# Kernel optimization log

Hardware: AMD Instinct MI355X
Metric: run time of the kernel (lower is better)

The kernel has to match this reference:

```python
import jax, jax.numpy as jnp
import numpy as np

IN_FEATS = 602
N_HIDDEN = 256
N_CLASSES = 41
N_SRC0 = 292864   # block-1 src nodes (2-hop neighborhood)
N_DST0 = 11264    # block-1 dst == block-0 src (1-hop neighborhood)
N_DST1 = 1024     # seeds
FAN0 = 25         # neighbors per dst in block applied by layer 0
FAN1 = 10         # neighbors per dst in block applied by layer 1


def setup_inputs() -> dict:
    key = jax.random.key(0)
    ks = jax.random.split(key, 9)
    x = jax.random.normal(ks[0], (N_SRC0, IN_FEATS), dtype=jnp.float32)
    src_idx0 = jax.random.randint(ks[1], (N_DST0 * FAN0,), 0, N_SRC0)
    src_idx1 = jax.random.randint(ks[2], (N_DST1 * FAN1,), 0, N_DST0)
    s0 = 1.0 / np.sqrt(IN_FEATS)
    s1 = 1.0 / np.sqrt(N_HIDDEN)
    W_self0 = jax.random.uniform(ks[3], (IN_FEATS, N_HIDDEN), jnp.float32, -s0, s0)
    W_neigh0 = jax.random.uniform(ks[4], (IN_FEATS, N_HIDDEN), jnp.float32, -s0, s0)
    b0 = jnp.zeros((N_HIDDEN,), jnp.float32)
    W_self1 = jax.random.uniform(ks[5], (N_HIDDEN, N_CLASSES), jnp.float32, -s1, s1)
    W_neigh1 = jax.random.uniform(ks[6], (N_HIDDEN, N_CLASSES), jnp.float32, -s1, s1)
    b1 = jnp.zeros((N_CLASSES,), jnp.float32)
    return {"x": x, "W_self0": W_self0, "W_neigh0": W_neigh0, "b0": b0,
            "W_self1": W_self1, "W_neigh1": W_neigh1, "b1": b1,
            "src_idx0": src_idx0, "src_idx1": src_idx1}


def _sage_layer(h_src, h_dst, src_idx, fanout, W_self, W_neigh, b):
    # mean aggregation over exactly `fanout` sampled neighbors per dst node
    n_dst = h_dst.shape[0]
    h_neigh = h_src[src_idx].reshape(n_dst, fanout, -1).mean(axis=1)
    return h_dst @ W_self + h_neigh @ W_neigh + b


def reference(x, W_self0, W_neigh0, b0, W_self1, W_neigh1, b1, src_idx0, src_idx1):
    # layer 0: [N_SRC0, in] -> [N_DST0, hidden], relu; dropout is identity (eval mode)
    h = jax.nn.relu(_sage_layer(x, x[:N_DST0], src_idx0, FAN0, W_self0, W_neigh0, b0))
    # layer 1: [N_DST0, hidden] -> [N_DST1, classes], no activation
    out = _sage_layer(h, h[:N_DST1], src_idx1, FAN1, W_self1, W_neigh1, b1)
    return out
```

## Files before the change

### kernel.cpp

```cpp
#include <hip/hip_runtime.h>
#include <hip/hip_bf16.h>

#define IN_FEATS 602
#define N_HIDDEN 256
#define N_CLASSES 41
#define N_SRC0 292864
#define N_DST0 11264
#define N_DST1 1024
#define FAN0 25
#define FAN1 10
#define KPAD 1216

typedef __attribute__((ext_vector_type(4))) float f32x4;
typedef __attribute__((ext_vector_type(8))) short bf16x8;

static __device__ __forceinline__ unsigned pack_bf16x2(float lo, float hi) {
    unsigned a = __float_as_uint(lo);
    unsigned b = __float_as_uint(hi);
    a = (a + 0x7fffu + ((a >> 16) & 1u)) >> 16;
    b = (b + 0x7fffu + ((b >> 16) & 1u)) >> 16;
    return (a & 0xffffu) | (b << 16);
}

__global__ __launch_bounds__(256) void agg0_kernel(
    const float* __restrict__ x,
    const int* __restrict__ idx,
    __hip_bfloat16* __restrict__ A)
{
    const int wave = threadIdx.x >> 6;
    const int lane = threadIdx.x & 63;
    const int d = blockIdx.x * 4 + wave;

    __shared__ int sidx[4][FAN0];
    if (lane < FAN0) sidx[wave][lane] = idx[d * FAN0 + lane];
    __syncthreads();

    unsigned* Aself  = (unsigned*)(A + (size_t)d * KPAD);
    const float* xself = x + (size_t)d * IN_FEATS;

    if (lane < 6) Aself[602 + lane] = 0u;

    #pragma unroll
    for (int p = 0; p < 5; ++p) {
        const int f2 = p * 64 + lane;
        if (f2 > 300) break;
        const int f = f2 * 2;
        float sx = 0.f, sy = 0.f;
        #pragma unroll
        for (int n = 0; n < FAN0; ++n) {
            const float2 v = *(const float2*)&x[(size_t)sidx[wave][n] * IN_FEATS + f];
            sx += v.x; sy += v.y;
        }
        const float2 s = *(const float2*)&xself[f];
        Aself[f2] = pack_bf16x2(s.x, s.y);
        ((unsigned*)((__hip_bfloat16*)Aself + IN_FEATS))[f2] =
            pack_bf16x2(sx * (1.0f / FAN0), sy * (1.0f / FAN0));
    }
}

__global__ __launch_bounds__(256) void wprep_kernel(
    const float* __restrict__ Ws,
    const float* __restrict__ Wn,
    __hip_bfloat16* __restrict__ Wt)
{
    __shared__ float tile[32][33];
    const int k0 = blockIdx.x * 32, n0 = blockIdx.y * 32;
    const int tx = threadIdx.x & 31, ty = threadIdx.x >> 5;

    #pragma unroll
    for (int i = 0; i < 4; ++i) {
        const int k = k0 + ty + i * 8;
        const int n = n0 + tx;
        float v = 0.f;
        if (k < IN_FEATS)            v = Ws[(size_t)k * N_HIDDEN + n];
        else if (k < 2 * IN_FEATS)   v = Wn[(size_t)(k - IN_FEATS) * N_HIDDEN + n];
        tile[ty + i * 8][tx] = v;
    }
    __syncthreads();
    #pragma unroll
    for (int i = 0; i < 4; ++i) {
        const int n = n0 + ty + i * 8;
        const int k = k0 + tx;
        Wt[(size_t)n * KPAD + k] = __float2bfloat16(tile[tx][ty + i * 8]);
    }
}

#define BKK 64
#define LDSW 72

__global__ __launch_bounds__(256) void gemm0_mfma(
    const __hip_bfloat16* __restrict__ A,
    const __hip_bfloat16* __restrict__ Wt,
    const float* __restrict__ bias,
    float* __restrict__ h)
{
    __shared__ __hip_bfloat16 As[64 * LDSW];
    __shared__ __hip_bfloat16 Bs[64 * LDSW];

    const int tid  = threadIdx.x;
    const int lane = tid & 63;
    const int wave = tid >> 6;
    const int wm = wave >> 1, wn = wave & 1;
    const int g = lane >> 4, r = lane & 15;
    const int m0 = blockIdx.y * 64, n0 = blockIdx.x * 64;

    const int srow = tid >> 2;
    const int sc   = (tid & 3) * 16;

    const size_t a_off = (size_t)(m0 + srow) * KPAD + sc;
    const size_t b_off = (size_t)(n0 + srow) * KPAD + sc;

    f32x4 acc[2][2] = {};

    for (int k0 = 0; k0 < KPAD; k0 += BKK) {
        *(float4*)&As[srow * LDSW + sc]     = *(const float4*)&A[a_off + k0];
        *(float4*)&As[srow * LDSW + sc + 8] = *(const float4*)&A[a_off + k0 + 8];
        *(float4*)&Bs[srow * LDSW + sc]     = *(const float4*)&Wt[b_off + k0];
        *(float4*)&Bs[srow * LDSW + sc + 8] = *(const float4*)&Wt[b_off + k0 + 8];
        __syncthreads();

        #pragma unroll
        for (int kh = 0; kh < 2; ++kh) {
            const bf16x8 af0 = *(const bf16x8*)&As[(wm * 32 +      r) * LDSW + kh * 32 + g * 8];
            const bf16x8 af1 = *(const bf16x8*)&As[(wm * 32 + 16 + r) * LDSW + kh * 32 + g * 8];
            const bf16x8 bf0 = *(const bf16x8*)&Bs[(wn * 32 +      r) * LDSW + kh * 32 + g * 8];
            const bf16x8 bf1 = *(const bf16x8*)&Bs[(wn * 32 + 16 + r) * LDSW + kh * 32 + g * 8];

            acc[0][0] = __builtin_amdgcn_mfma_f32_16x16x32_bf16(af0, bf0, acc[0][0], 0, 0, 0);
            acc[0][1] = __builtin_amdgcn_mfma_f32_16x16x32_bf16(af0, bf1, acc[0][1], 0, 0, 0);
            acc[1][0] = __builtin_amdgcn_mfma_f32_16x16x32_bf16(af1, bf0, acc[1][0], 0, 0, 0);
            acc[1][1] = __builtin_amdgcn_mfma_f32_16x16x32_bf16(af1, bf1, acc[1][1], 0, 0, 0);
        }
        __syncthreads();
    }

    #pragma unroll
    for (int mh = 0; mh < 2; ++mh)
        #pragma unroll
        for (int nh = 0; nh < 2; ++nh) {
            const int col = n0 + wn * 32 + nh * 16 + r;
            const float bv = bias[col];
            #pragma unroll
            for (int j = 0; j < 4; ++j) {
                const int row = m0 + wm * 32 + mh * 16 + g * 4 + j;
                const float v = acc[mh][nh][j] + bv;
                h[(size_t)row * N_HIDDEN + col] = fmaxf(v, 0.f);
            }
        }
}

__global__ __launch_bounds__(64) void tail_kernel(
    const float* __restrict__ h,
    const int* __restrict__ idx1,
    const float* __restrict__ Ws,
    const float* __restrict__ Wn,
    const float* __restrict__ b,
    float* __restrict__ out)
{
    const int d = blockIdx.x;
    __shared__ float hd[N_HIDDEN];
    __shared__ float hn[N_HIDDEN];
    __shared__ int sidx[FAN1];
    if (threadIdx.x < FAN1) sidx[threadIdx.x] = idx1[d * FAN1 + threadIdx.x];
    __syncthreads();

    for (int k = threadIdx.x; k < N_HIDDEN; k += 64) {
        hd[k] = h[(size_t)d * N_HIDDEN + k];
        float a = 0.f;
        #pragma unroll
        for (int i = 0; i < FAN1; ++i)
            a += h[(size_t)sidx[i] * N_HIDDEN + k];
        hn[k] = a * (1.0f / FAN1);
    }
    __syncthreads();

    if (threadIdx.x < N_CLASSES) {
        const int n = threadIdx.x;
        float a0 = b[n], a1 = 0.f, a2 = 0.f, a3 = 0.f;
        #pragma unroll 4
        for (int k = 0; k < N_HIDDEN; k += 4) {
            a0 += hd[k + 0] * Ws[(k + 0) * N_CLASSES + n] + hn[k + 0] * Wn[(k + 0) * N_CLASSES + n];
            a1 += hd[k + 1] * Ws[(k + 1) * N_CLASSES + n] + hn[k + 1] * Wn[(k + 1) * N_CLASSES + n];
            a2 += hd[k + 2] * Ws[(k + 2) * N_CLASSES + n] + hn[k + 2] * Wn[(k + 2) * N_CLASSES + n];
            a3 += hd[k + 3] * Ws[(k + 3) * N_CLASSES + n] + hn[k + 3] * Wn[(k + 3) * N_CLASSES + n];
        }
        out[(size_t)d * N_CLASSES + n] = a0 + a1 + a2 + a3;
    }
}

extern "C" void kernel_launch(void* const* d_in, const int* in_sizes, int n_in,
                              void* d_out, int out_size, void* d_ws, size_t ws_size,
                              hipStream_t stream) {
    const float* x       = (const float*)d_in[0];
    const float* Wself0  = (const float*)d_in[1];
    const float* Wneigh0 = (const float*)d_in[2];
    const float* b0      = (const float*)d_in[3];
    const float* Wself1  = (const float*)d_in[4];
    const float* Wneigh1 = (const float*)d_in[5];
    const float* b1      = (const float*)d_in[6];
    const int*   idx0    = (const int*)d_in[7];
    const int*   idx1    = (const int*)d_in[8];
    float* out = (float*)d_out;

    __hip_bfloat16* Abf = (__hip_bfloat16*)d_ws;
    __hip_bfloat16* Wt  = Abf + (size_t)N_DST0 * KPAD;
    float*          h   = (float*)(Wt + (size_t)N_HIDDEN * KPAD);

    wprep_kernel<<<dim3(KPAD / 32, N_HIDDEN / 32), 256, 0, stream>>>(Wself0, Wneigh0, Wt);
    agg0_kernel<<<N_DST0 / 4, 256, 0, stream>>>(x, idx0, Abf);
    gemm0_mfma<<<dim3(N_HIDDEN / 64, N_DST0 / 64), 256, 0, stream>>>(Abf, Wt, b0, h);
    tail_kernel<<<N_DST1, 64, 0, stream>>>(h, idx1, Wself1, Wneigh1, b1, out);
}
```

Measured before the change: 231.3 us.

## Fuse neighbor aggregation into layer-0 GEMM via LDS-resident A tile

Merges the gather/mean aggregation kernel and the MFMA GEMM into one kernel. Each block aggregates 16 destination rows into an LDS bf16 tile, then each wave computes 64 output columns, streaming the weight fragments directly from global memory with register double-buffering. This removes the round trip of the bf16 A matrix through global memory and one launch. In exchange, every block re-reads the full 1216x256 weight matrix from L2, and 704 blocks each doing serial gather work may limit latency hiding.

```diff
diff --git a/kernel.cpp b/kernel.cpp
--- a/kernel.cpp
+++ b/kernel.cpp
@@ -10,6 +10,8 @@
 #define FAN0 25
 #define FAN1 10
 #define KPAD 1216
+#define MT 16
+#define ALDS 1224
 
 typedef __attribute__((ext_vector_type(4))) float f32x4;
 typedef __attribute__((ext_vector_type(8))) short bf16x8;
@@ -20,42 +22,6 @@
     a = (a + 0x7fffu + ((a >> 16) & 1u)) >> 16;
     b = (b + 0x7fffu + ((b >> 16) & 1u)) >> 16;
     return (a & 0xffffu) | (b << 16);
-}
-
-__global__ __launch_bounds__(256) void agg0_kernel(
-    const float* __restrict__ x,
-    const int* __restrict__ idx,
-    __hip_bfloat16* __restrict__ A)
-{
-    const int wave = threadIdx.x >> 6;
-    const int lane = threadIdx.x & 63;
-    const int d = blockIdx.x * 4 + wave;
-
-    __shared__ int sidx[4][FAN0];
-    if (lane < FAN0) sidx[wave][lane] = idx[d * FAN0 + lane];
-    __syncthreads();
-
-    unsigned* Aself  = (unsigned*)(A + (size_t)d * KPAD);
-    const float* xself = x + (size_t)d * IN_FEATS;
-
-    if (lane < 6) Aself[602 + lane] = 0u;
-
-    #pragma unroll
-    for (int p = 0; p < 5; ++p) {
-        const int f2 = p * 64 + lane;
-        if (f2 > 300) break;
-        const int f = f2 * 2;
-        float sx = 0.f, sy = 0.f;
-        #pragma unroll
-        for (int n = 0; n < FAN0; ++n) {
-            const float2 v = *(const float2*)&x[(size_t)sidx[wave][n] * IN_FEATS + f];
-            sx += v.x; sy += v.y;
-        }
-        const float2 s = *(const float2*)&xself[f];
-        Aself[f2] = pack_bf16x2(s.x, s.y);
-        ((unsigned*)((__hip_bfloat16*)Aself + IN_FEATS))[f2] =
-            pack_bf16x2(sx * (1.0f / FAN0), sy * (1.0f / FAN0));
-    }
 }
 
 __global__ __launch_bounds__(256) void wprep_kernel(
@@ -85,68 +51,91 @@
     }
 }
 
-#define BKK 64
-#define LDSW 72
-
-__global__ __launch_bounds__(256) void gemm0_mfma(
-    const __hip_bfloat16* __restrict__ A,
+__global__ __launch_bounds__(256) void fused0_kernel(
+    const float* __restrict__ x,
+    const int* __restrict__ idx0,
     const __hip_bfloat16* __restrict__ Wt,
     const float* __restrict__ bias,
     float* __restrict__ h)
 {
-    __shared__ __hip_bfloat16 As[64 * LDSW];
-    __shared__ __hip_bfloat16 Bs[64 * LDSW];
+    __shared__ __hip_bfloat16 Atile[MT][ALDS];
 
     const int tid  = threadIdx.x;
     const int lane = tid & 63;
-    const int wave = tid >> 6;
-    const int wm = wave >> 1, wn = wave & 1;
-    const int g = lane >> 4, r = lane & 15;
-    const int m0 = blockIdx.y * 64, n0 = blockIdx.x * 64;
-
-    const int srow = tid >> 2;
-    const int sc   = (tid & 3) * 16;
-
-    const size_t a_off = (size_t)(m0 + srow) * KPAD + sc;
-    const size_t b_off = (size_t)(n0 + srow) * KPAD + sc;
-
-    f32x4 acc[2][2] = {};
-
-    for (int k0 = 0; k0 < KPAD; k0 += BKK) {
-        *(float4*)&As[srow * LDSW + sc]     = *(const float4*)&A[a_off + k0];
-        *(float4*)&As[srow * LDSW + sc + 8] = *(const float4*)&A[a_off + k0 + 8];
-        *(float4*)&Bs[srow * LDSW + sc]     = *(const float4*)&Wt[b_off + k0];
-        *(float4*)&Bs[srow * LDSW + sc + 8] = *(const float4*)&Wt[b_off + k0 + 8];
-        __syncthreads();
-
-        #pragma unroll
-        for (int kh = 0; kh < 2; ++kh) {
-            const bf16x8 af0 = *(const bf16x8*)&As[(wm * 32 +      r) * LDSW + kh * 32 + g * 8];
-            const bf16x8 af1 = *(const bf16x8*)&As[(wm * 32 + 16 + r) * LDSW + kh * 32 + g * 8];
-            const bf16x8 bf0 = *(const bf16x8*)&Bs[(wn * 32 +      r) * LDSW + kh * 32 + g * 8];
-            const bf16x8 bf1 = *(const bf16x8*)&Bs[(wn * 32 + 16 + r) * LDSW + kh * 32 + g * 8];
-
-            acc[0][0] = __builtin_amdgcn_mfma_f32_16x16x32_bf16(af0, bf0, acc[0][0], 0, 0, 0);
-            acc[0][1] = __builtin_amdgcn_mfma_f32_16x16x32_bf16(af0, bf1, acc[0][1], 0, 0, 0);
-            acc[1][0] = __builtin_amdgcn_mfma_f32_16x16x32_bf16(af1, bf0, acc[1][0], 0, 0, 0);
-            acc[1][1] = __builtin_amdgcn_mfma_f32_16x16x32_bf16(af1, bf1, acc[1][1], 0, 0, 0);
-        }
-        __syncthreads();
-    }
-
-    #pragma unroll
-    for (int mh = 0; mh < 2; ++mh)
-        #pragma unroll
-        for (int nh = 0; nh < 2; ++nh) {
-            const int col = n0 + wn * 32 + nh * 16 + r;
-            const float bv = bias[col];
-            #pragma unroll
-            for (int j = 0; j < 4; ++j) {
-                const int row = m0 + wm * 32 + mh * 16 + g * 4 + j;
-                const float v = acc[mh][nh][j] + bv;
-                h[(size_t)row * N_HIDDEN + col] = fmaxf(v, 0.f);
+    const int w    = tid >> 6;
+    const int r    = lane & 15;
+    const int g    = lane >> 4;
+
+    #pragma unroll
+    for (int s = 0; s < 4; ++s) {
+        const int local = w * 4 + s;
+        const int d = blockIdx.x * MT + local;
+        const int* ip = idx0 + d * FAN0;
+
+        int ridx[FAN0];
+        #pragma unroll
+        for (int n = 0; n < FAN0; ++n)
+            ridx[n] = __builtin_amdgcn_readfirstlane(ip[n]);
+
+        if (lane < 10)
+            *(unsigned*)((char*)&Atile[local][0] + 2408 + lane * 4) = 0u;
+
+        #pragma unroll
+        for (int p = 0; p < 5; ++p) {
+            const int f2 = p * 64 + lane;
+            if (f2 <= 300) {
+                const int f = f2 * 2;
+                float sx = 0.f, sy = 0.f;
+                #pragma unroll
+                for (int n = 0; n < FAN0; ++n) {
+                    const float2 v = *(const float2*)&x[(size_t)ridx[n] * IN_FEATS + f];
+                    sx += v.x; sy += v.y;
+                }
+                const float2 sv = *(const float2*)&x[(size_t)d * IN_FEATS + f];
+                *(unsigned*)((char*)&Atile[local][0] + f2 * 4) = pack_bf16x2(sv.x, sv.y);
+                *(unsigned*)((char*)&Atile[local][0] + 1204 + f2 * 4) =
+                    pack_bf16x2(sx * (1.0f / FAN0), sy * (1.0f / FAN0));
             }
         }
+    }
+    __syncthreads();
+
+    const int cb = w * 64;
+    f32x4 acc[4] = {};
+
+#define LOADB(T, B) { _Pragma("unroll") \
+    for (int nf = 0; nf < 4; ++nf) \
+        B[nf] = *(const bf16x8*)&Wt[(size_t)(cb + nf * 16 + r) * KPAD + (T) * 32 + g * 8]; }
+#define DOMFMA(T, B) { \
+    const bf16x8 af = *(const bf16x8*)&Atile[r][(T) * 32 + g * 8]; \
+    _Pragma("unroll") \
+    for (int nf = 0; nf < 4; ++nf) \
+        acc[nf] = __builtin_amdgcn_mfma_f32_16x16x32_bf16(af, B[nf], acc[nf], 0, 0, 0); }
+
+    bf16x8 bA[4], bB[4];
+    LOADB(0, bA)
+    for (int t = 0; t < 36; t += 2) {
+        LOADB(t + 1, bB)
+        DOMFMA(t, bA)
+        LOADB(t + 2, bA)
+        DOMFMA(t + 1, bB)
+    }
+    LOADB(37, bB)
+    DOMFMA(36, bA)
+    DOMFMA(37, bB)
+#undef LOADB
+#undef DOMFMA
+
+    #pragma unroll
+    for (int nf = 0; nf < 4; ++nf) {
+        const int col = cb + nf * 16 + r;
+        const float bv = bias[col];
+        #pragma unroll
+        for (int j = 0; j < 4; ++j) {
+            const int row = blockIdx.x * MT + g * 4 + j;
+            h[(size_t)row * N_HIDDEN + col] = fmaxf(acc[nf][j] + bv, 0.f);
+        }
+    }
 }
 
 __global__ __launch_bounds__(64) void tail_kernel(
@@ -202,12 +191,10 @@
     const int*   idx1    = (const int*)d_in[8];
     float* out = (float*)d_out;
 
-    __hip_bfloat16* Abf = (__hip_bfloat16*)d_ws;
-    __hip_bfloat16* Wt  = Abf + (size_t)N_DST0 * KPAD;
-    float*          h   = (float*)(Wt + (size_t)N_HIDDEN * KPAD);
+    __hip_bfloat16* Wt = (__hip_bfloat16*)d_ws;
+    float*          h  = (float*)(Wt + (size_t)N_HIDDEN * KPAD);
 
     wprep_kernel<<<dim3(KPAD / 32, N_HIDDEN / 32), 256, 0, stream>>>(Wself0, Wneigh0, Wt);
-    agg0_kernel<<<N_DST0 / 4, 256, 0, stream>>>(x, idx0, Abf);
-    gemm0_mfma<<<dim3(N_HIDDEN / 64, N_DST0 / 64), 256, 0, stream>>>(Abf, Wt, b0, h);
+    fused0_kernel<<<N_DST0 / MT, 256, 0, stream>>>(x, idx0, Wt, b0, h);
     tail_kernel<<<N_DST1, 64, 0, stream>>>(h, idx1, Wself1, Wneigh1, b1, out);
 }
```

Result: slower. 243.2 us (+5.1%).

## Overlap chunked aggregation with GEMM via role-dispatched combo kernel

Applied to the files above, without the earlier changes.

Splits the layer-0 destination nodes into four chunks and launches a combined kernel whose blocks either prep weights, run the MFMA GEMM on the previous chunk, or aggregate the next chunk. The memory-bound gather then runs concurrently with the compute-bound GEMM in a software pipeline across launches. The tail kernel is also repacked to four destinations per 256-thread block with float4 gathers. The cost is extra launches and a shared LDS buffer sized for the largest role, which may reduce occupancy for the aggregation blocks.

```diff
diff --git a/kernel.cpp b/kernel.cpp
--- a/kernel.cpp
+++ b/kernel.cpp
@@ -10,6 +10,12 @@
 #define FAN0 25
 #define FAN1 10
 #define KPAD 1216
+#define LDSW 72
+#define NCHUNK 4
+#define CH (N_DST0 / NCHUNK)
+#define NW ((KPAD / 32) * 8)
+#define NGC (4 * (CH / 64))
+#define NAC (CH / 4)
 
 typedef __attribute__((ext_vector_type(4))) float f32x4;
 typedef __attribute__((ext_vector_type(8))) short bf16x8;
@@ -22,49 +28,16 @@
     return (a & 0xffffu) | (b << 16);
 }
 
-__global__ __launch_bounds__(256) void agg0_kernel(
-    const float* __restrict__ x,
-    const int* __restrict__ idx,
-    __hip_bfloat16* __restrict__ A)
-{
-    const int wave = threadIdx.x >> 6;
-    const int lane = threadIdx.x & 63;
-    const int d = blockIdx.x * 4 + wave;
-
-    __shared__ int sidx[4][FAN0];
-    if (lane < FAN0) sidx[wave][lane] = idx[d * FAN0 + lane];
-    __syncthreads();
-
-    unsigned* Aself  = (unsigned*)(A + (size_t)d * KPAD);
-    const float* xself = x + (size_t)d * IN_FEATS;
-
-    if (lane < 6) Aself[602 + lane] = 0u;
-
-    #pragma unroll
-    for (int p = 0; p < 5; ++p) {
-        const int f2 = p * 64 + lane;
-        if (f2 > 300) break;
-        const int f = f2 * 2;
-        float sx = 0.f, sy = 0.f;
-        #pragma unroll
-        for (int n = 0; n < FAN0; ++n) {
-            const float2 v = *(const float2*)&x[(size_t)sidx[wave][n] * IN_FEATS + f];
-            sx += v.x; sy += v.y;
-        }
-        const float2 s = *(const float2*)&xself[f];
-        Aself[f2] = pack_bf16x2(s.x, s.y);
-        ((unsigned*)((__hip_bfloat16*)Aself + IN_FEATS))[f2] =
-            pack_bf16x2(sx * (1.0f / FAN0), sy * (1.0f / FAN0));
-    }
-}
-
-__global__ __launch_bounds__(256) void wprep_kernel(
-    const float* __restrict__ Ws,
-    const float* __restrict__ Wn,
+#define SMBYTES (2 * 64 * LDSW * 2)
+
+static __device__ __forceinline__ void wprep_role(
+    int b, char* sm,
+    const float* __restrict__ Ws, const float* __restrict__ Wn,
     __hip_bfloat16* __restrict__ Wt)
 {
-    __shared__ float tile[32][33];
-    const int k0 = blockIdx.x * 32, n0 = blockIdx.y * 32;
+    float (*tile)[33] = (float(*)[33])sm;
+    const int k0 = (b % (KPAD / 32)) * 32;
+    const int n0 = (b / (KPAD / 32)) * 32;
     const int tx = threadIdx.x & 31, ty = threadIdx.x >> 5;
 
     #pragma unroll
@@ -85,24 +58,61 @@
     }
 }
 
-#define BKK 64
-#define LDSW 72
-
-__global__ __launch_bounds__(256) void gemm0_mfma(
+static __device__ __forceinline__ void agg_role(
+    int b, int dst0, char* sm,
+    const float* __restrict__ x,
+    const int* __restrict__ idx0,
+    __hip_bfloat16* __restrict__ A)
+{
+    int (*sidx)[FAN0] = (int(*)[FAN0])sm;
+    const int wave = threadIdx.x >> 6;
+    const int lane = threadIdx.x & 63;
+    const int d = dst0 + b * 4 + wave;
+
+    if (lane < FAN0) sidx[wave][lane] = idx0[d * FAN0 + lane];
+    __syncthreads();
+
+    unsigned* Aself = (unsigned*)(A + (size_t)d * KPAD);
+    const float* xself = x + (size_t)d * IN_FEATS;
+
+    if (lane < 6) Aself[602 + lane] = 0u;
+
+    #pragma unroll
+    for (int p = 0; p < 5; ++p) {
+        const int f2 = p * 64 + lane;
+        if (f2 <= 300) {
+            const int f = f2 * 2;
+            float sx = 0.f, sy = 0.f;
+            #pragma unroll
+            for (int n = 0; n < FAN0; ++n) {
+                const float2 v = *(const float2*)&x[(size_t)sidx[wave][n] * IN_FEATS + f];
+                sx += v.x; sy += v.y;
+            }
+            const float2 sv = *(const float2*)&xself[f];
+            *(unsigned*)((char*)Aself + f2 * 4) = pack_bf16x2(sv.x, sv.y);
+            *(unsigned*)((char*)Aself + 1204 + f2 * 4) =
+                pack_bf16x2(sx * (1.0f / FAN0), sy * (1.0f / FAN0));
+        }
+    }
+}
+
+static __device__ __forceinline__ void gemm_role(
+    int b, int dst0, char* sm,
     const __hip_bfloat16* __restrict__ A,
     const __hip_bfloat16* __restrict__ Wt,
     const float* __restrict__ bias,
     float* __restrict__ h)
 {
-    __shared__ __hip_bfloat16 As[64 * LDSW];
-    __shared__ __hip_bfloat16 Bs[64 * LDSW];
+    short* As = (short*)sm;
+    short* Bs = As + 64 * LDSW;
 
     const int tid  = threadIdx.x;
     const int lane = tid & 63;
     const int wave = tid >> 6;
     const int wm = wave >> 1, wn = wave & 1;
     const int g = lane >> 4, r = lane & 15;
-    const int m0 = blockIdx.y * 64, n0 = blockIdx.x * 64;
+    const int n0 = (b & 3) * 64;
+    const int m0 = dst0 + (b >> 2) * 64;
 
     const int srow = tid >> 2;
     const int sc   = (tid & 3) * 16;
@@ -112,7 +122,7 @@
 
     f32x4 acc[2][2] = {};
 
-    for (int k0 = 0; k0 < KPAD; k0 += BKK) {
+    for (int k0 = 0; k0 < KPAD; k0 += 64) {
         *(float4*)&As[srow * LDSW + sc]     = *(const float4*)&A[a_off + k0];
         *(float4*)&As[srow * LDSW + sc + 8] = *(const float4*)&A[a_off + k0 + 8];
         *(float4*)&Bs[srow * LDSW + sc]     = *(const float4*)&Wt[b_off + k0];
@@ -143,13 +153,32 @@
             #pragma unroll
             for (int j = 0; j < 4; ++j) {
                 const int row = m0 + wm * 32 + mh * 16 + g * 4 + j;
-                const float v = acc[mh][nh][j] + bv;
-                h[(size_t)row * N_HIDDEN + col] = fmaxf(v, 0.f);
+                h[(size_t)row * N_HIDDEN + col] = fmaxf(acc[mh][nh][j] + bv, 0.f);
             }
         }
 }
 
-__global__ __launch_bounds__(64) void tail_kernel(
+__global__ __launch_bounds__(256) void combo_kernel(
+    const float* __restrict__ x,
+    const int* __restrict__ idx0,
+    const float* __restrict__ Ws0,
+    const float* __restrict__ Wn0,
+    const float* __restrict__ b0,
+    __hip_bfloat16* __restrict__ A,
+    __hip_bfloat16* __restrict__ Wt,
+    float* __restrict__ h,
+    int nw, int ng, int gemm_dst0, int agg_dst0)
+{
+    __shared__ __align__(16) char sm[SMBYTES];
+    int b = blockIdx.x;
+    if (b < nw) { wprep_role(b, sm, Ws0, Wn0, Wt); return; }
+    b -= nw;
+    if (b < ng) { gemm_role(b, gemm_dst0, sm, A, Wt, b0, h); return; }
+    b -= ng;
+    agg_role(b, agg_dst0, sm, x, idx0, A);
+}
+
+__global__ __launch_bounds__(256) void tail_kernel(
     const float* __restrict__ h,
     const int* __restrict__ idx1,
     const float* __restrict__ Ws,
@@ -157,32 +186,42 @@
     const float* __restrict__ b,
     float* __restrict__ out)
 {
-    const int d = blockIdx.x;
-    __shared__ float hd[N_HIDDEN];
-    __shared__ float hn[N_HIDDEN];
-    __shared__ int sidx[FAN1];
-    if (threadIdx.x < FAN1) sidx[threadIdx.x] = idx1[d * FAN1 + threadIdx.x];
-    __syncthreads();
-
-    for (int k = threadIdx.x; k < N_HIDDEN; k += 64) {
-        hd[k] = h[(size_t)d * N_HIDDEN + k];
-        float a = 0.f;
+    const int w = threadIdx.x >> 6;
+    const int lane = threadIdx.x & 63;
+    const int d = blockIdx.x * 4 + w;
+
+    __shared__ float hd[4][N_HIDDEN];
+    __shared__ float hn[4][N_HIDDEN];
+    __shared__ int sidx[4][FAN1];
+    if (lane < FAN1) sidx[w][lane] = idx1[d * FAN1 + lane];
+    __syncthreads();
+
+    {
+        const int k0 = lane * 4;
+        const float4 self = *(const float4*)&h[(size_t)d * N_HIDDEN + k0];
+        float ax = 0.f, ay = 0.f, az = 0.f, aw = 0.f;
         #pragma unroll
-        for (int i = 0; i < FAN1; ++i)
-            a += h[(size_t)sidx[i] * N_HIDDEN + k];
-        hn[k] = a * (1.0f / FAN1);
-    }
-    __syncthreads();
-
-    if (threadIdx.x < N_CLASSES) {
-        const int n = threadIdx.x;
+        for (int i = 0; i < FAN1; ++i) {
+            const float4 v = *(const float4*)&h[(size_t)sidx[w][i] * N_HIDDEN + k0];
+            ax += v.x; ay += v.y; az += v.z; aw += v.w;
+        }
+        *(float4*)&hd[w][k0] = self;
+        hn[w][k0 + 0] = ax * (1.0f / FAN1);
+        hn[w][k0 + 1] = ay * (1.0f / FAN1);
+        hn[w][k0 + 2] = az * (1.0f / FAN1);
+        hn[w][k0 + 3] = aw * (1.0f / FAN1);
+    }
+    __syncthreads();
+
+    if (lane < N_CLASSES) {
+        const int n = lane;
         float a0 = b[n], a1 = 0.f, a2 = 0.f, a3 = 0.f;
         #pragma unroll 4
         for (int k = 0; k < N_HIDDEN; k += 4) {
-            a0 += hd[k + 0] * Ws[(k + 0) * N_CLASSES + n] + hn[k + 0] * Wn[(k + 0) * N_CLASSES + n];
-            a1 += hd[k + 1] * Ws[(k + 1) * N_CLASSES + n] + hn[k + 1] * Wn[(k + 1) * N_CLASSES + n];
-            a2 += hd[k + 2] * Ws[(k + 2) * N_CLASSES + n] + hn[k + 2] * Wn[(k + 2) * N_CLASSES + n];
-            a3 += hd[k + 3] * Ws[(k + 3) * N_CLASSES + n] + hn[k + 3] * Wn[(k + 3) * N_CLASSES + n];
+            a0 += hd[w][k + 0] * Ws[(k + 0) * N_CLASSES + n] + hn[w][k + 0] * Wn[(k + 0) * N_CLASSES + n];
+            a1 += hd[w][k + 1] * Ws[(k + 1) * N_CLASSES + n] + hn[w][k + 1] * Wn[(k + 1) * N_CLASSES + n];
+            a2 += hd[w][k + 2] * Ws[(k + 2) * N_CLASSES + n] + hn[w][k + 2] * Wn[(k + 2) * N_CLASSES + n];
+            a3 += hd[w][k + 3] * Ws[(k + 3) * N_CLASSES + n] + hn[w][k + 3] * Wn[(k + 3) * N_CLASSES + n];
         }
         out[(size_t)d * N_CLASSES + n] = a0 + a1 + a2 + a3;
     }
@@ -202,12 +241,17 @@
     const int*   idx1    = (const int*)d_in[8];
     float* out = (float*)d_out;
 
-    __hip_bfloat16* Abf = (__hip_bfloat16*)d_ws;
-    __hip_bfloat16* Wt  = Abf + (size_t)N_DST0 * KPAD;
-    float*          h   = (float*)(Wt + (size_t)N_HIDDEN * KPAD);
-
-    wprep_kernel<<<dim3(KPAD / 32, N_HIDDEN / 32), 256, 0, stream>>>(Wself0, Wneigh0, Wt);
-    agg0_kernel<<<N_DST0 / 4, 256, 0, stream>>>(x, idx0, Abf);
-    gemm0_mfma<<<dim3(N_HIDDEN / 64, N_DST0 / 64), 256, 0, stream>>>(Abf, Wt, b0, h);
-    tail_kernel<<<N_DST1, 64, 0, stream>>>(h, idx1, Wself1, Wneigh1, b1, out);
-}
+    __hip_bfloat16* A  = (__hip_bfloat16*)d_ws;
+    __hip_bfloat16* Wt = A + (size_t)N_DST0 * KPAD;
+    float*          h  = (float*)(Wt + (size_t)N_HIDDEN * KPAD);
+
+    combo_kernel<<<NW + NAC, 256, 0, stream>>>(
+        x, idx0, Wself0, Wneigh0, b0, A, Wt, h, NW, 0, 0, 0);
+    for (int c = 1; c < NCHUNK; ++c)
+        combo_kernel<<<NGC + NAC, 256, 0, stream>>>(
+            x, idx0, Wself0, Wneigh0, b0, A, Wt, h,
+            0, NGC, (c - 1) * CH, c * CH);
+    combo_kernel<<<NGC, 256, 0, stream>>>(
+        x, idx0, Wself0, Wneigh0, b0, A, Wt, h, 0, NGC, (NCHUNK - 1) * CH, 0);
+    tail_kernel<<<N_DST1 / 4, 256, 0, stream>>>(h, idx1, Wself1, Wneigh1, b1, out);
+}
```

Result: slower. 238.5 us (+3.1%).
